# Performance work log

Measured on AMD Instinct MI355X. Metric: run time of the kernel, lower is better.

Reference implementation:

```python
import jax, jax.numpy as jnp
import numpy as np

N, C, H, W = 8, 80, 200, 200
PRE_NMS_THRESH = 0.05
PRE_NMS_TOP_N = 1000
NMS_THRESH = 0.6
FPN_POST_NMS_TOP_N = 100
MIN_SIZE = 0.0
TO_REMOVE = 1.0
CLASS_OFFSET = 100000.0  # > any coordinate; separates classes for class-aware NMS


def setup_inputs() -> dict:
    key = jax.random.key(0)
    k1, k2, k3, k4, k5 = jax.random.split(key, 5)
    # logits shifted so sigmoid probs sit near the 0.05 threshold (realistic sparsity)
    box_cls = jax.random.normal(k1, (N, C, H, W), jnp.float32) - 3.0
    box_regression = jax.random.uniform(k2, (N, 4, H, W), jnp.float32) * 64.0
    centerness = jax.random.normal(k3, (N, 1, H, W), jnp.float32)
    locations = jax.random.uniform(k4, (H * W, 2), jnp.float32) * 1600.0
    image_sizes = jax.random.randint(k5, (N, 2), 800, 1600, jnp.int32)  # (h, w)
    return {"locations": locations, "box_cls": box_cls,
            "box_regression": box_regression, "centerness": centerness,
            "image_sizes": image_sizes}


def _pairwise_iou(boxes):
    x1, y1, x2, y2 = boxes[:, 0], boxes[:, 1], boxes[:, 2], boxes[:, 3]
    area = (x2 - x1 + TO_REMOVE) * (y2 - y1 + TO_REMOVE)  # [K]
    iw = jnp.clip(jnp.minimum(x2[:, None], x2[None, :]) - jnp.maximum(x1[:, None], x1[None, :]) + TO_REMOVE, 0.0)
    ih = jnp.clip(jnp.minimum(y2[:, None], y2[None, :]) - jnp.maximum(y1[:, None], y1[None, :]) + TO_REMOVE, 0.0)
    inter = iw * ih
    return inter / (area[:, None] + area[None, :] - inter)


def reference(locations, box_cls, box_regression, centerness, image_sizes):
    n, c, h, w = box_cls.shape
    # [N,C,H,W] -> [N,HW,C] probs; [N,4,H,W] -> [N,HW,4]; centerness -> [N,HW]
    cls_prob = jax.nn.sigmoid(box_cls.transpose(0, 2, 3, 1).reshape(n, -1, c))
    reg = box_regression.transpose(0, 2, 3, 1).reshape(n, -1, 4)
    cent = jax.nn.sigmoid(centerness.transpose(0, 2, 3, 1).reshape(n, -1))

    def per_image(p, r, ct, hw):
        # candidate mask on raw class probs (before centerness weighting), as in source
        cand = p > PRE_NMS_THRESH                      # [HW, C]
        scores = p * ct[:, None]                       # [HW, C]
        flat = jnp.where(cand, scores, -jnp.inf).reshape(-1)
        top_s, top_i = jax.lax.top_k(flat, PRE_NMS_TOP_N)   # sorted desc
        loc_idx = top_i // c
        labels = top_i % c + 1
        valid = top_s > 0.0
        l2 = locations[loc_idx]                        # [K, 2]
        rr = r[loc_idx]                                # [K, 4]
        boxes = jnp.concatenate([l2 - rr[:, :2], l2 + rr[:, 2:]], axis=-1)
        ih = hw[0].astype(jnp.float32)
        iw = hw[1].astype(jnp.float32)
        boxes = jnp.stack([jnp.clip(boxes[:, 0], 0.0, iw - 1.0),
                           jnp.clip(boxes[:, 1], 0.0, ih - 1.0),
                           jnp.clip(boxes[:, 2], 0.0, iw - 1.0),
                           jnp.clip(boxes[:, 3], 0.0, ih - 1.0)], axis=-1)
        bw = boxes[:, 2] - boxes[:, 0] + TO_REMOVE
        bh = boxes[:, 3] - boxes[:, 1] + TO_REMOVE
        valid = valid & (bw >= MIN_SIZE) & (bh >= MIN_SIZE)
        # class-aware NMS via per-class coordinate offset
        ob = boxes + labels.astype(jnp.float32)[:, None] * CLASS_OFFSET
        iou = _pairwise_iou(ob)                        # [K, K]
        K = PRE_NMS_TOP_N
        idxs = jnp.arange(K)
        def body(supp, i):
            keep_i = valid[i] & jnp.logical_not(supp[i])
            supp = supp | (keep_i & (iou[i] > NMS_THRESH) & (idxs != i))
            return supp, keep_i
        _, keep = jax.lax.scan(body, jnp.zeros(K, dtype=bool), idxs)
        fscores = jnp.where(keep & valid, top_s, -jnp.inf)
        fs, fi = jax.lax.top_k(fscores, FPN_POST_NMS_TOP_N)
        fv = fs > 0.0
        fb = boxes[fi] * fv[:, None].astype(boxes.dtype)
        fl = jnp.where(fv, labels[fi], 0).astype(jnp.float32)
        out_s = jnp.where(fv, jnp.sqrt(jnp.where(fv, fs, 1.0)), 0.0)  # sqrt of cls*centerness
        # [K_post, 6] = x1,y1,x2,y2,score,label
        return jnp.concatenate([fb, out_s[:, None], fl[:, None]], axis=-1)

    return jax.vmap(per_image)(cls_prob, reg, cent, image_sizes)
```

## Files before the change

kernel.cpp:

```cpp
#include <hip/hip_runtime.h>
#include <math.h>

#define NIMG 8
#define NCLS 80
#define HW 40000
#define M (NCLS*HW)
#define UBINS 4096
#define CANDL 4096
#define SPILL_CAP 65536
#define BCAP 1024
#define TOPK 1000
#define OUTK 100
#define PRE_T 0.05f
#define NMS_T 0.6f
#define FLOOR_S 0.25f
#define FLOOR_BITS 0x3E800000u
#define FLOOR_SAFE 0.2494f

__device__ unsigned int       g_scnt[NIMG][32];
__device__ unsigned int       g_ovf[NIMG];
__device__ float              g_xthr[NIMG * HW];
__device__ float              g_sct[NIMG * HW];
__device__ unsigned long long g_key[NIMG][SPILL_CAP];

__device__ __forceinline__ float sigmoid_exact(float x){
    return 1.0f / (1.0f + expf(-x));
}

__global__ void k0_init(const float* __restrict__ cent){
    int t = blockIdx.x * blockDim.x + threadIdx.x;
    if (t < NIMG * 32) ((unsigned int*)g_scnt)[t] = 0u;
    if (t < NIMG) g_ovf[t] = 0u;
    if (t < NIMG * HW){
        float pct = sigmoid_exact(cent[t]);
        g_sct[t] = pct;
        float a = FLOOR_SAFE / pct;
        float xt;
        if (a >= 1.0f) xt = 3.0e38f;
        else {
            float am = fminf(a, 0.98f);
            xt = logf(am / (1.0f - am));
        }
        g_xthr[t] = xt;
    }
}

__global__ void __launch_bounds__(1024) k1_spill(const float* __restrict__ cls){
    const int n   = blockIdx.y;
    const int tid = threadIdx.x;
    const int e0  = blockIdx.x * 4096 + tid * 4;
    __shared__ unsigned long long skey[BCAP];
    __shared__ unsigned int lcnt, lbase;
    if (tid == 0) lcnt = 0u;
    __syncthreads();
    if (e0 < M){
        const int c  = e0 / HW;
        const int hw = e0 - c * HW;
        float4 x  = *(const float4*)(cls + (size_t)n * M + e0);
        float4 th = *(const float4*)(g_xthr + n * HW + hw);
        #define SPILL1(J, XV) \
        if (XV >= (J==0?th.x:J==1?th.y:J==2?th.z:th.w)){ \
            float p_ = sigmoid_exact(XV); \
            if (p_ > PRE_T){ \
                float s_ = p_ * g_sct[n * HW + hw + J]; \
                unsigned long long key_ = ((unsigned long long)__float_as_uint(s_) << 32) \
                    | (unsigned long long)(0xFFFFFFFFu - (unsigned int)((hw + J) * NCLS + c)); \
                unsigned int pp_ = atomicAdd(&lcnt, 1u); \
                if (pp_ < BCAP) skey[pp_] = key_; \
            } \
        }
        SPILL1(0, x.x)
        SPILL1(1, x.y)
        SPILL1(2, x.z)
        SPILL1(3, x.w)
        #undef SPILL1
    }
    __syncthreads();
    unsigned int raw = lcnt;
    unsigned int cnt = raw < BCAP ? raw : BCAP;
    if (tid == 0){
        lbase = cnt ? atomicAdd(&g_scnt[n][0], cnt) : 0u;
        if (raw > BCAP) g_ovf[n] = 1u;
    }
    __syncthreads();
    unsigned int base = lbase;
    for (unsigned int i = tid; i < cnt; i += 1024){
        unsigned int pos = base + i;
        if (pos < SPILL_CAP) g_key[n][pos] = skey[i];
    }
}

struct SelPhase {
    unsigned int hist[UBINS];
    unsigned int cs[256];
    unsigned long long keysL[CANDL];
};
struct NmsPhase {
    float ox1[TOPK], oy1[TOPK], ox2[TOPK], oy2[TOPK], oar[TOPK];
    float bxs[TOPK][4];
    float sc[TOPK];
    int   lab[TOPK];
    int   keeplist[OUTK];
    unsigned int  Wc[16][80];
    unsigned int  coff[81];
    unsigned int  wcnt[16];
    unsigned short ord[1024];
    unsigned char validf[TOPK];
    unsigned char supp[TOPK];
    unsigned char keepf[1024];
};
union KU { SelPhase sel; NmsPhase nms; };

__global__ void __launch_bounds__(1024) k2_select_nms(const float* __restrict__ cls,
                                                      const float* __restrict__ loc,
                                                      const float* __restrict__ reg,
                                                      const int*   __restrict__ imsz,
                                                      float* __restrict__ out){
    const int n = blockIdx.x;
    const int tid = threadIdx.x;
    const int lane = tid & 63;
    const int wv   = tid >> 6;
    __shared__ KU u;
    __shared__ unsigned long long stop[TOPK];
    __shared__ unsigned int lcnt, c025, s_cut, s_flag, s_nmsfb, s_cnt;

    for (int i = tid; i < UBINS; i += 1024) u.sel.hist[i] = 0u;
    if (tid == 0){ lcnt = 0u; c025 = 0u; s_nmsfb = 0u; }
    if (tid < TOPK) stop[tid] = 0ull;
    __syncthreads();

    unsigned int scnt_raw = g_scnt[n][0];
    unsigned int S = scnt_raw < SPILL_CAP ? scnt_raw : SPILL_CAP;

    for (unsigned int i = tid; i < S; i += 1024){
        unsigned long long k = g_key[n][i];
        unsigned int bits = (unsigned int)(k >> 32);
        float s = __uint_as_float(bits);
        int bin = (int)(s * 4096.0f);
        atomicAdd(&u.sel.hist[bin], 1u);
        unsigned long long mb = __ballot(bits >= FLOOR_BITS);
        if (lane == 0 && mb) atomicAdd(&c025, (unsigned int)__popcll(mb));
    }
    __syncthreads();
    if (tid < 256){
        unsigned int s = 0;
        int base = tid * 16;
        #pragma unroll
        for (int i = 0; i < 16; ++i) s += u.sel.hist[base + i];
        u.sel.cs[tid] = s;
    }
    __syncthreads();
    if (tid == 0){
        unsigned int acc = 0; int cut = 0;
        int c = 255;
        for (; c >= 0; --c){ if (acc + u.sel.cs[c] >= TOPK) break; acc += u.sel.cs[c]; }
        unsigned int Cest = 0;
        if (c >= 0){
            int b = c*16 + 15;
            for (;; --b){
                if (acc + u.sel.hist[b] >= TOPK || b == c*16){ cut = b; break; }
                acc += u.sel.hist[b];
            }
            Cest = acc + u.sel.hist[cut];
        }
        unsigned int fl = (scnt_raw > SPILL_CAP) || g_ovf[n] || (c < 0) ||
                          (c025 < TOPK) || (Cest > CANDL) ? 1u : 0u;
        s_cut = (unsigned int)cut; s_flag = fl;
    }
    __syncthreads();

    if (s_flag){
        for (int i = tid; i < UBINS; i += 1024) u.sel.hist[i] = 0u;
        __syncthreads();
        const float* cls_n = cls + (size_t)n * M;
        const float* sct_n = g_sct + n * HW;
        for (int e = tid; e < M; e += 1024){
            float p = sigmoid_exact(cls_n[e]);
            if (p > PRE_T){
                int c = e / HW; int hw = e - c * HW;
                float s = p * sct_n[hw];
                atomicAdd(&u.sel.hist[(int)(s * 4096.0f)], 1u);
            }
        }
        __syncthreads();
        if (tid < 256){
            unsigned int s = 0;
            int base = tid * 16;
            #pragma unroll
            for (int i = 0; i < 16; ++i) s += u.sel.hist[base + i];
            u.sel.cs[tid] = s;
        }
        __syncthreads();
        if (tid == 0){
            unsigned int acc = 0; int cut = 0; int c = 255;
            for (; c >= 0; --c){ if (acc + u.sel.cs[c] >= TOPK) break; acc += u.sel.cs[c]; }
            if (c >= 0){
                int b = c*16 + 15;
                for (;; --b){ acc += u.sel.hist[b]; if (acc >= TOPK || b == c*16) break; }
                cut = b;
            }
            while (acc > CANDL && cut < UBINS){ acc -= u.sel.hist[cut]; cut++; }
            s_cut = (unsigned int)cut;
        }
        __syncthreads();
        unsigned int cutb = s_cut;
        for (int e = tid; e < M; e += 1024){
            float p = sigmoid_exact(cls_n[e]);
            if (p > PRE_T){
                int c = e / HW; int hw = e - c * HW;
                float s = p * sct_n[hw];
                if ((int)(s * 4096.0f) >= (int)cutb){
                    unsigned int pos = atomicAdd(&lcnt, 1u);
                    if (pos < CANDL){
                        unsigned int idx = (unsigned int)(hw * NCLS + c);
                        u.sel.keysL[pos] = ((unsigned long long)__float_as_uint(s) << 32)
                                         | (unsigned long long)(0xFFFFFFFFu - idx);
                    }
                }
            }
        }
    } else {
        unsigned int cutb = s_cut;
        for (unsigned int i = tid; i < S; i += 1024){
            unsigned long long k = g_key[n][i];
            float s = __uint_as_float((unsigned int)(k >> 32));
            bool pass = ((unsigned int)(int)(s * 4096.0f)) >= cutb;
            unsigned long long mb = __ballot(pass);
            unsigned int wcnt_ = (unsigned int)__popcll(mb);
            unsigned int base = 0;
            if (lane == 0 && wcnt_) base = atomicAdd(&lcnt, wcnt_);
            base = (unsigned int)__builtin_amdgcn_readfirstlane((int)base);
            if (pass){
                unsigned int p = base + (unsigned int)__popcll(mb & ((1ull << lane) - 1ull));
                if (p < CANDL) u.sel.keysL[p] = k;
            }
        }
    }
    __syncthreads();

    int C = (int)(lcnt < CANDL ? lcnt : CANDL);
    if (C <= 2048){
        int Nsort = (C <= 1024) ? 1024 : 2048;
        for (int i = C + tid; i < Nsort; i += 1024) u.sel.keysL[i] = 0ull;
        __syncthreads();
        for (int k = 2; k <= Nsort; k <<= 1){
            for (int j = k >> 1; j > 0; j >>= 1){
                if (tid < (Nsort >> 1)){
                    int i  = ((tid & ~(j - 1)) << 1) | (tid & (j - 1));
                    int p2 = i | j;
                    unsigned long long a = u.sel.keysL[i];
                    unsigned long long b = u.sel.keysL[p2];
                    bool up = ((i & k) == 0);
                    if (up ? (a < b) : (a > b)){ u.sel.keysL[i] = b; u.sel.keysL[p2] = a; }
                }
                __syncthreads();
            }
        }
        if (tid < TOPK) stop[tid] = u.sel.keysL[tid];
    } else {
        for (int i = tid; i < C; i += 1024){
            unsigned long long k = u.sel.keysL[i];
            int rank = 0;
            for (int j = 0; j < C; ++j) rank += (u.sel.keysL[j] > k) ? 1 : 0;
            if (rank < TOPK) stop[rank] = k;
        }
    }
    __syncthreads();

    float rx1 = 0.f, ry1 = 0.f, rx2 = -1.f, ry2 = -1.f, rar = 1.f;
    float ihh = (float)imsz[2*n + 0];
    float iww = (float)imsz[2*n + 1];
    unsigned long long kk = (tid < TOPK) ? stop[tid] : 0ull;
    __syncthreads();

    u.nms.keepf[tid] = 0;
    { unsigned int* wz = &u.nms.Wc[0][0];
      for (int i = tid; i < 16*80; i += 1024) wz[i] = 0u; }

    if (tid < TOPK){
        unsigned int bits = (unsigned int)(kk >> 32);
        float s = __uint_as_float(bits);
        u.nms.supp[tid] = 0;
        if (s > 0.0f){
            unsigned int idx = 0xFFFFFFFFu - (unsigned int)(kk & 0xFFFFFFFFull);
            int hw = (int)(idx / NCLS);
            int c  = (int)(idx % NCLS);
            int l  = c + 1;
            float x  = loc[2*hw], y = loc[2*hw + 1];
            float r0 = reg[((size_t)n*4 + 0)*HW + hw];
            float r1 = reg[((size_t)n*4 + 1)*HW + hw];
            float r2 = reg[((size_t)n*4 + 2)*HW + hw];
            float r3 = reg[((size_t)n*4 + 3)*HW + hw];
            float x1 = fminf(fmaxf(x - r0, 0.0f), iww - 1.0f);
            float y1 = fminf(fmaxf(y - r1, 0.0f), ihh - 1.0f);
            float x2 = fminf(fmaxf(x + r2, 0.0f), iww - 1.0f);
            float y2 = fminf(fmaxf(y + r3, 0.0f), ihh - 1.0f);
            u.nms.bxs[tid][0] = x1; u.nms.bxs[tid][1] = y1;
            u.nms.bxs[tid][2] = x2; u.nms.bxs[tid][3] = y2;
            float off = (float)l * 100000.0f;
            float a1 = x1 + off, b1 = y1 + off, a2 = x2 + off, b2 = y2 + off;
            float ar = (a2 - a1 + 1.0f) * (b2 - b1 + 1.0f);
            u.nms.ox1[tid] = a1; u.nms.oy1[tid] = b1;
            u.nms.ox2[tid] = a2; u.nms.oy2[tid] = b2; u.nms.oar[tid] = ar;
            rx1 = a1; ry1 = b1; rx2 = a2; ry2 = b2; rar = ar;
            u.nms.sc[tid] = s; u.nms.lab[tid] = l; u.nms.validf[tid] = 1;
        } else {
            u.nms.validf[tid] = 0; u.nms.sc[tid] = 0.0f; u.nms.lab[tid] = 0;
            u.nms.bxs[tid][0] = u.nms.bxs[tid][1] = 0.0f;
            u.nms.bxs[tid][2] = u.nms.bxs[tid][3] = 0.0f;
            u.nms.ox1[tid] = 0.f; u.nms.oy1[tid] = 0.f;
            u.nms.ox2[tid] = -1.f; u.nms.oy2[tid] = -1.f; u.nms.oar[tid] = 1.f;
        }
    }
    __syncthreads();

    int mk = -1;
    if (tid < TOPK && u.nms.validf[tid]) mk = u.nms.lab[tid] - 1;
    if (mk >= 0) atomicAdd(&u.nms.Wc[wv][mk], 1u);
    __syncthreads();
    if (tid < NCLS){
        unsigned int acc = 0;
        for (int w = 0; w < 16; ++w){
            unsigned int v = u.nms.Wc[w][tid];
            u.nms.Wc[w][tid] = acc;
            acc += v;
        }
        u.nms.coff[tid] = acc;
        if (acc > 64) atomicOr(&s_nmsfb, 1u);
    }
    __syncthreads();
    if (tid == 0){
        unsigned int acc = 0;
        for (int k = 0; k < NCLS; ++k){ unsigned int t = u.nms.coff[k]; u.nms.coff[k] = acc; acc += t; }
        u.nms.coff[NCLS] = acc;
    }
    __syncthreads();

    if (!s_nmsfb){
        int below = 0;
        for (int l = 0; l < 64; ++l){
            int ok = __shfl(mk, l);
            below += (l < lane && ok == mk) ? 1 : 0;
        }
        if (mk >= 0){
            unsigned int pos = u.nms.coff[mk] + u.nms.Wc[wv][mk] + (unsigned int)below;
            u.nms.ord[pos] = (unsigned short)tid;
        }
        __syncthreads();

        for (int k = wv; k < NCLS; k += 16){
            int base = (int)u.nms.coff[k];
            int ck   = (int)u.nms.coff[k + 1] - base;
            if (ck <= 0) continue;
            int rr = (lane < ck) ? (int)u.nms.ord[base + lane] : -1;
            float bx1 = 0.f, by1 = 0.f, bx2 = -1.f, by2 = -1.f, bar = 1.f;
            if (rr >= 0){
                bx1 = u.nms.ox1[rr]; by1 = u.nms.oy1[rr];
                bx2 = u.nms.ox2[rr]; by2 = u.nms.oy2[rr]; bar = u.nms.oar[rr];
            }
            int sup = 0;
            for (int p = 0; p < ck; ++p){
                int keep_p = !__shfl(sup, p);
                if (keep_p){
                    float px1 = __shfl(bx1, p), py1 = __shfl(by1, p);
                    float px2 = __shfl(bx2, p), py2 = __shfl(by2, p);
                    float par = __shfl(bar, p);
                    if (lane > p && rr >= 0){
                        float ix1 = fmaxf(px1, bx1);
                        float iy1 = fmaxf(py1, by1);
                        float ix2 = fminf(px2, bx2);
                        float iy2 = fminf(py2, by2);
                        float iw_ = fmaxf(ix2 - ix1 + 1.0f, 0.0f);
                        float ih_ = fmaxf(iy2 - iy1 + 1.0f, 0.0f);
                        float inter = iw_ * ih_;
                        float iou = inter / (par + bar - inter);
                        if (iou > NMS_T) sup = 1;
                    }
                }
            }
            if (rr >= 0) u.nms.keepf[rr] = sup ? 0 : 1;
        }
        __syncthreads();

        int kf = (int)u.nms.keepf[tid];
        unsigned long long mb = __ballot(kf != 0);
        if (lane == 0) u.nms.wcnt[wv] = (unsigned int)__popcll(mb);
        __syncthreads();
        if (tid == 0){
            unsigned int acc = 0;
            for (int w = 0; w < 16; ++w){ unsigned int t = u.nms.wcnt[w]; u.nms.wcnt[w] = acc; acc += t; }
            s_cnt = acc < OUTK ? acc : OUTK;
        }
        __syncthreads();
        if (kf){
            unsigned int slot = u.nms.wcnt[wv] + (unsigned int)__popcll(mb & ((1ull << lane) - 1ull));
            if (slot < OUTK) u.nms.keeplist[slot] = tid;
        }
    } else {
        int cnt = 0;
        for (int i = 0; i < TOPK; ++i){
            bool keep_i = u.nms.validf[i] && !u.nms.supp[i];
            if (keep_i){
                if (tid == 0) u.nms.keeplist[cnt] = i;
                if (tid < TOPK && tid != i){
                    float ix1 = fmaxf(u.nms.ox1[i], rx1);
                    float iy1 = fmaxf(u.nms.oy1[i], ry1);
                    float ix2 = fminf(u.nms.ox2[i], rx2);
                    float iy2 = fminf(u.nms.oy2[i], ry2);
                    float iw_ = fmaxf(ix2 - ix1 + 1.0f, 0.0f);
                    float ih_ = fmaxf(iy2 - iy1 + 1.0f, 0.0f);
                    float inter = iw_ * ih_;
                    float iou = inter / (u.nms.oar[i] + rar - inter);
                    if (iou > NMS_T) u.nms.supp[tid] = 1;
                }
                cnt++;
                __syncthreads();
                if (cnt == OUTK) break;
            }
        }
        if (tid == 0) s_cnt = (unsigned int)(cnt < OUTK ? cnt : OUTK);
    }
    __syncthreads();

    int cnt = (int)s_cnt;
    if (tid < OUTK){
        float r0=0.f,r1=0.f,r2=0.f,r3=0.f,r4=0.f,r5=0.f;
        if (tid < cnt){
            int i = u.nms.keeplist[tid];
            r0 = u.nms.bxs[i][0]; r1 = u.nms.bxs[i][1];
            r2 = u.nms.bxs[i][2]; r3 = u.nms.bxs[i][3];
            r4 = sqrtf(u.nms.sc[i]); r5 = (float)u.nms.lab[i];
        }
        float* o = out + ((size_t)n*OUTK + tid)*6;
        o[0]=r0; o[1]=r1; o[2]=r2; o[3]=r3; o[4]=r4; o[5]=r5;
    }
}

extern "C" void kernel_launch(void* const* d_in, const int* in_sizes, int n_in,
                              void* d_out, int out_size, void* d_ws, size_t ws_size,
                              hipStream_t stream){
    const float* loc  = (const float*)d_in[0];
    const float* cls  = (const float*)d_in[1];
    const float* reg  = (const float*)d_in[2];
    const float* cent = (const float*)d_in[3];
    const int*   imsz = (const int*)d_in[4];
    float* out = (float*)d_out;

    hipLaunchKernelGGL(k0_init,       dim3(625),                 dim3(512),  0, stream, cent);
    hipLaunchKernelGGL(k1_spill,      dim3((M+4095)/4096, NIMG), dim3(1024), 0, stream, cls);
    hipLaunchKernelGGL(k2_select_nms, dim3(NIMG),                dim3(1024), 0, stream,
                       cls, loc, reg, imsz, out);
}
```

Baseline: 257.4 us.

## Add direct register bitonic sort fast path and wave-aggregated spill

The spill kernel drops its per-block shared-memory staging and instead uses wave ballots with one global atomic per wave, writing keys straight to the global buffer. The select kernel gains a fast path: when the spill count is between 1000 and 2048 with no overflow, it sorts all spilled keys directly using a bitonic sort that does the small strides with register shuffles and only the larger strides in shared memory. This skips the histogram and cut passes whenever the 1000th key still clears the floor. Several serial single-thread prefix scans are also replaced with parallel or shuffle-based scans. The cost is more global atomics in the spill kernel and extra shuffle work, in exchange for fewer barriers and fewer passes over the keys.

```diff
diff --git a/kernel.cpp b/kernel.cpp
--- a/kernel.cpp
+++ b/kernel.cpp
@@ -8,7 +8,6 @@
 #define UBINS 4096
 #define CANDL 4096
 #define SPILL_CAP 65536
-#define BCAP 1024
 #define TOPK 1000
 #define OUTK 100
 #define PRE_T 0.05f
@@ -25,6 +24,12 @@
 
 __device__ __forceinline__ float sigmoid_exact(float x){
     return 1.0f / (1.0f + expf(-x));
+}
+
+__device__ __forceinline__ unsigned long long shfl_xor_u64(unsigned long long v, int j){
+    int lo = __shfl_xor((int)(unsigned int)(v & 0xffffffffull), j);
+    int hi = __shfl_xor((int)(unsigned int)(v >> 32), j);
+    return ((unsigned long long)(unsigned int)hi << 32) | (unsigned long long)(unsigned int)lo;
 }
 
 __global__ void k0_init(const float* __restrict__ cent){
@@ -46,48 +51,43 @@
 }
 
 __global__ void __launch_bounds__(1024) k1_spill(const float* __restrict__ cls){
-    const int n   = blockIdx.y;
-    const int tid = threadIdx.x;
-    const int e0  = blockIdx.x * 4096 + tid * 4;
-    __shared__ unsigned long long skey[BCAP];
-    __shared__ unsigned int lcnt, lbase;
-    if (tid == 0) lcnt = 0u;
-    __syncthreads();
-    if (e0 < M){
-        const int c  = e0 / HW;
-        const int hw = e0 - c * HW;
-        float4 x  = *(const float4*)(cls + (size_t)n * M + e0);
-        float4 th = *(const float4*)(g_xthr + n * HW + hw);
-        #define SPILL1(J, XV) \
-        if (XV >= (J==0?th.x:J==1?th.y:J==2?th.z:th.w)){ \
+    const int n    = blockIdx.y;
+    const int tid  = threadIdx.x;
+    const int lane = tid & 63;
+    const int e0   = blockIdx.x * 4096 + tid * 4;
+    if (e0 >= M) return;
+    const int c  = e0 / HW;
+    const int hw = e0 - c * HW;
+    float4 x  = *(const float4*)(cls + (size_t)n * M + e0);
+    float4 th = *(const float4*)(g_xthr + n * HW + hw);
+    #define SPILLW(J, XV, TH) { \
+        bool cd2 = false; unsigned long long key_ = 0ull; \
+        if (XV >= TH){ \
             float p_ = sigmoid_exact(XV); \
             if (p_ > PRE_T){ \
                 float s_ = p_ * g_sct[n * HW + hw + J]; \
-                unsigned long long key_ = ((unsigned long long)__float_as_uint(s_) << 32) \
-                    | (unsigned long long)(0xFFFFFFFFu - (unsigned int)((hw + J) * NCLS + c)); \
-                unsigned int pp_ = atomicAdd(&lcnt, 1u); \
-                if (pp_ < BCAP) skey[pp_] = key_; \
+                key_ = ((unsigned long long)__float_as_uint(s_) << 32) \
+                     | (unsigned long long)(0xFFFFFFFFu - (unsigned int)((hw + J) * NCLS + c)); \
+                cd2 = true; \
             } \
-        }
-        SPILL1(0, x.x)
-        SPILL1(1, x.y)
-        SPILL1(2, x.z)
-        SPILL1(3, x.w)
-        #undef SPILL1
-    }
-    __syncthreads();
-    unsigned int raw = lcnt;
-    unsigned int cnt = raw < BCAP ? raw : BCAP;
-    if (tid == 0){
-        lbase = cnt ? atomicAdd(&g_scnt[n][0], cnt) : 0u;
-        if (raw > BCAP) g_ovf[n] = 1u;
-    }
-    __syncthreads();
-    unsigned int base = lbase;
-    for (unsigned int i = tid; i < cnt; i += 1024){
-        unsigned int pos = base + i;
-        if (pos < SPILL_CAP) g_key[n][pos] = skey[i];
-    }
+        } \
+        unsigned long long mk_ = __ballot(cd2); \
+        if (mk_){ \
+            unsigned int base_ = 0; \
+            if (lane == 0) base_ = atomicAdd(&g_scnt[n][0], (unsigned int)__popcll(mk_)); \
+            base_ = (unsigned int)__builtin_amdgcn_readfirstlane((int)base_); \
+            if (cd2){ \
+                unsigned int pos_ = base_ + (unsigned int)__popcll(mk_ & ((1ull << lane) - 1ull)); \
+                if (pos_ < SPILL_CAP) g_key[n][pos_] = key_; \
+                else g_ovf[n] = 1u; \
+            } \
+        } \
+    }
+    SPILLW(0, x.x, th.x)
+    SPILLW(1, x.y, th.y)
+    SPILLW(2, x.z, th.z)
+    SPILLW(3, x.w, th.w)
+    #undef SPILLW
 }
 
 struct SelPhase {
@@ -102,6 +102,7 @@
     int   lab[TOPK];
     int   keeplist[OUTK];
     unsigned int  Wc[16][80];
+    unsigned int  ctot[80];
     unsigned int  coff[81];
     unsigned int  wcnt[16];
     unsigned short ord[1024];
@@ -110,6 +111,16 @@
     unsigned char keepf[1024];
 };
 union KU { SelPhase sel; NmsPhase nms; };
+
+#define REGSTEP(K_, J_) { \
+    unsigned long long pa = shfl_xor_u64(va, (J_)); \
+    unsigned long long pb = shfl_xor_u64(vb, (J_)); \
+    bool fa = ((tid & (J_)) == 0); \
+    bool da = ((tid & (K_)) == 0); \
+    bool db = (((tid + 1024) & (K_)) == 0); \
+    va = (fa == da) ? (va > pa ? va : pa) : (va < pa ? va : pa); \
+    vb = (fa == db) ? (vb > pb ? vb : pb) : (vb < pb ? vb : pb); \
+}
 
 __global__ void __launch_bounds__(1024) k2_select_nms(const float* __restrict__ cls,
                                                       const float* __restrict__ loc,
@@ -122,65 +133,69 @@
     const int wv   = tid >> 6;
     __shared__ KU u;
     __shared__ unsigned long long stop[TOPK];
-    __shared__ unsigned int lcnt, c025, s_cut, s_flag, s_nmsfb, s_cnt;
-
-    for (int i = tid; i < UBINS; i += 1024) u.sel.hist[i] = 0u;
-    if (tid == 0){ lcnt = 0u; c025 = 0u; s_nmsfb = 0u; }
-    if (tid < TOPK) stop[tid] = 0ull;
-    __syncthreads();
+    __shared__ unsigned int lcnt, c025, s_cut, s_flag, s_nmsfb, s_cnt, s_aok;
+
+    if (tid == 0){ s_nmsfb = 0u; }
 
     unsigned int scnt_raw = g_scnt[n][0];
+    unsigned int ovf_f    = g_ovf[n];
     unsigned int S = scnt_raw < SPILL_CAP ? scnt_raw : SPILL_CAP;
 
-    for (unsigned int i = tid; i < S; i += 1024){
-        unsigned long long k = g_key[n][i];
-        unsigned int bits = (unsigned int)(k >> 32);
-        float s = __uint_as_float(bits);
-        int bin = (int)(s * 4096.0f);
-        atomicAdd(&u.sel.hist[bin], 1u);
-        unsigned long long mb = __ballot(bits >= FLOOR_BITS);
-        if (lane == 0 && mb) atomicAdd(&c025, (unsigned int)__popcll(mb));
-    }
-    __syncthreads();
-    if (tid < 256){
-        unsigned int s = 0;
-        int base = tid * 16;
-        #pragma unroll
-        for (int i = 0; i < 16; ++i) s += u.sel.hist[base + i];
-        u.sel.cs[tid] = s;
-    }
-    __syncthreads();
-    if (tid == 0){
-        unsigned int acc = 0; int cut = 0;
-        int c = 255;
-        for (; c >= 0; --c){ if (acc + u.sel.cs[c] >= TOPK) break; acc += u.sel.cs[c]; }
-        unsigned int Cest = 0;
-        if (c >= 0){
-            int b = c*16 + 15;
-            for (;; --b){
-                if (acc + u.sel.hist[b] >= TOPK || b == c*16){ cut = b; break; }
-                acc += u.sel.hist[b];
-            }
-            Cest = acc + u.sel.hist[cut];
-        }
-        unsigned int fl = (scnt_raw > SPILL_CAP) || g_ovf[n] || (c < 0) ||
-                          (c025 < TOPK) || (Cest > CANDL) ? 1u : 0u;
-        s_cut = (unsigned int)cut; s_flag = fl;
-    }
-    __syncthreads();
-
-    if (s_flag){
+    bool modeA = (!ovf_f) && (scnt_raw >= TOPK) && (scnt_raw <= 2048);
+    unsigned long long kk = 0ull;
+    bool needBC = true;
+
+    if (modeA){
+        unsigned long long va = ((unsigned int)tid < S) ? g_key[n][tid] : 0ull;
+        unsigned long long vb = ((unsigned int)(tid + 1024) < S) ? g_key[n][tid + 1024] : 0ull;
+
+        REGSTEP(2,1)
+        REGSTEP(4,2)  REGSTEP(4,1)
+        REGSTEP(8,4)  REGSTEP(8,2)  REGSTEP(8,1)
+        REGSTEP(16,8) REGSTEP(16,4) REGSTEP(16,2) REGSTEP(16,1)
+        REGSTEP(32,16) REGSTEP(32,8) REGSTEP(32,4) REGSTEP(32,2) REGSTEP(32,1)
+        REGSTEP(64,32) REGSTEP(64,16) REGSTEP(64,8) REGSTEP(64,4) REGSTEP(64,2) REGSTEP(64,1)
+
+        for (int k = 128; k <= 2048; k <<= 1){
+            if (k == 2048){
+                unsigned long long mx = va > vb ? va : vb;
+                unsigned long long mn = va > vb ? vb : va;
+                va = mx; vb = mn;
+            }
+            u.sel.keysL[tid] = va; u.sel.keysL[tid + 1024] = vb;
+            __syncthreads();
+            for (int j = (k == 2048) ? 512 : (k >> 1); j >= 64; j >>= 1){
+                int i  = ((tid & ~(j - 1)) << 1) | (tid & (j - 1));
+                int l  = i | j;
+                unsigned long long a = u.sel.keysL[i];
+                unsigned long long b = u.sel.keysL[l];
+                bool up = ((i & k) == 0);
+                if (up ? (a < b) : (a > b)){ u.sel.keysL[i] = b; u.sel.keysL[l] = a; }
+                __syncthreads();
+            }
+            va = u.sel.keysL[tid]; vb = u.sel.keysL[tid + 1024];
+            REGSTEP(k,32) REGSTEP(k,16) REGSTEP(k,8) REGSTEP(k,4) REGSTEP(k,2) REGSTEP(k,1)
+        }
+        if (tid == TOPK - 1) s_aok = (((unsigned int)(va >> 32)) >= FLOOR_BITS) ? 1u : 0u;
+        kk = (tid < TOPK) ? va : 0ull;
+        __syncthreads();
+        needBC = (s_aok == 0u);
+    }
+
+    if (needBC){
         for (int i = tid; i < UBINS; i += 1024) u.sel.hist[i] = 0u;
-        __syncthreads();
-        const float* cls_n = cls + (size_t)n * M;
-        const float* sct_n = g_sct + n * HW;
-        for (int e = tid; e < M; e += 1024){
-            float p = sigmoid_exact(cls_n[e]);
-            if (p > PRE_T){
-                int c = e / HW; int hw = e - c * HW;
-                float s = p * sct_n[hw];
-                atomicAdd(&u.sel.hist[(int)(s * 4096.0f)], 1u);
-            }
+        if (tid == 0){ lcnt = 0u; c025 = 0u; }
+        if (tid < TOPK) stop[tid] = 0ull;
+        __syncthreads();
+
+        for (unsigned int i = tid; i < S; i += 1024){
+            unsigned long long k = g_key[n][i];
+            unsigned int bits = (unsigned int)(k >> 32);
+            float s = __uint_as_float(bits);
+            int bin = (int)(s * 4096.0f);
+            atomicAdd(&u.sel.hist[bin], 1u);
+            unsigned long long mb = __ballot(bits >= FLOOR_BITS);
+            if (lane == 0 && mb) atomicAdd(&c025, (unsigned int)__popcll(mb));
         }
         __syncthreads();
         if (tid < 256){
@@ -192,86 +207,128 @@
         }
         __syncthreads();
         if (tid == 0){
-            unsigned int acc = 0; int cut = 0; int c = 255;
+            unsigned int acc = 0; int cut = 0;
+            int c = 255;
             for (; c >= 0; --c){ if (acc + u.sel.cs[c] >= TOPK) break; acc += u.sel.cs[c]; }
+            unsigned int Cest = 0;
             if (c >= 0){
                 int b = c*16 + 15;
-                for (;; --b){ acc += u.sel.hist[b]; if (acc >= TOPK || b == c*16) break; }
-                cut = b;
-            }
-            while (acc > CANDL && cut < UBINS){ acc -= u.sel.hist[cut]; cut++; }
-            s_cut = (unsigned int)cut;
-        }
-        __syncthreads();
-        unsigned int cutb = s_cut;
-        for (int e = tid; e < M; e += 1024){
-            float p = sigmoid_exact(cls_n[e]);
-            if (p > PRE_T){
-                int c = e / HW; int hw = e - c * HW;
-                float s = p * sct_n[hw];
-                if ((int)(s * 4096.0f) >= (int)cutb){
-                    unsigned int pos = atomicAdd(&lcnt, 1u);
-                    if (pos < CANDL){
-                        unsigned int idx = (unsigned int)(hw * NCLS + c);
-                        u.sel.keysL[pos] = ((unsigned long long)__float_as_uint(s) << 32)
-                                         | (unsigned long long)(0xFFFFFFFFu - idx);
+                for (;; --b){
+                    if (acc + u.sel.hist[b] >= TOPK || b == c*16){ cut = b; break; }
+                    acc += u.sel.hist[b];
+                }
+                Cest = acc + u.sel.hist[cut];
+            }
+            unsigned int fl = (scnt_raw > SPILL_CAP) || ovf_f || (c < 0) ||
+                              (c025 < TOPK) || (Cest > CANDL) ? 1u : 0u;
+            s_cut = (unsigned int)cut; s_flag = fl;
+        }
+        __syncthreads();
+
+        if (s_flag){
+            for (int i = tid; i < UBINS; i += 1024) u.sel.hist[i] = 0u;
+            __syncthreads();
+            const float* cls_n = cls + (size_t)n * M;
+            const float* sct_n = g_sct + n * HW;
+            for (int e = tid; e < M; e += 1024){
+                float p = sigmoid_exact(cls_n[e]);
+                if (p > PRE_T){
+                    int c = e / HW; int hw = e - c * HW;
+                    float s = p * sct_n[hw];
+                    atomicAdd(&u.sel.hist[(int)(s * 4096.0f)], 1u);
+                }
+            }
+            __syncthreads();
+            if (tid < 256){
+                unsigned int s = 0;
+                int base = tid * 16;
+                #pragma unroll
+                for (int i = 0; i < 16; ++i) s += u.sel.hist[base + i];
+                u.sel.cs[tid] = s;
+            }
+            __syncthreads();
+            if (tid == 0){
+                unsigned int acc = 0; int cut = 0; int c = 255;
+                for (; c >= 0; --c){ if (acc + u.sel.cs[c] >= TOPK) break; acc += u.sel.cs[c]; }
+                if (c >= 0){
+                    int b = c*16 + 15;
+                    for (;; --b){ acc += u.sel.hist[b]; if (acc >= TOPK || b == c*16) break; }
+                    cut = b;
+                }
+                while (acc > CANDL && cut < UBINS){ acc -= u.sel.hist[cut]; cut++; }
+                s_cut = (unsigned int)cut;
+            }
+            __syncthreads();
+            unsigned int cutb = s_cut;
+            for (int e = tid; e < M; e += 1024){
+                float p = sigmoid_exact(cls_n[e]);
+                if (p > PRE_T){
+                    int c = e / HW; int hw = e - c * HW;
+                    float s = p * sct_n[hw];
+                    if ((int)(s * 4096.0f) >= (int)cutb){
+                        unsigned int pos = atomicAdd(&lcnt, 1u);
+                        if (pos < CANDL){
+                            unsigned int idx = (unsigned int)(hw * NCLS + c);
+                            u.sel.keysL[pos] = ((unsigned long long)__float_as_uint(s) << 32)
+                                             | (unsigned long long)(0xFFFFFFFFu - idx);
+                        }
                     }
                 }
             }
-        }
-    } else {
-        unsigned int cutb = s_cut;
-        for (unsigned int i = tid; i < S; i += 1024){
-            unsigned long long k = g_key[n][i];
-            float s = __uint_as_float((unsigned int)(k >> 32));
-            bool pass = ((unsigned int)(int)(s * 4096.0f)) >= cutb;
-            unsigned long long mb = __ballot(pass);
-            unsigned int wcnt_ = (unsigned int)__popcll(mb);
-            unsigned int base = 0;
-            if (lane == 0 && wcnt_) base = atomicAdd(&lcnt, wcnt_);
-            base = (unsigned int)__builtin_amdgcn_readfirstlane((int)base);
-            if (pass){
-                unsigned int p = base + (unsigned int)__popcll(mb & ((1ull << lane) - 1ull));
-                if (p < CANDL) u.sel.keysL[p] = k;
-            }
-        }
-    }
-    __syncthreads();
-
-    int C = (int)(lcnt < CANDL ? lcnt : CANDL);
-    if (C <= 2048){
-        int Nsort = (C <= 1024) ? 1024 : 2048;
-        for (int i = C + tid; i < Nsort; i += 1024) u.sel.keysL[i] = 0ull;
-        __syncthreads();
-        for (int k = 2; k <= Nsort; k <<= 1){
-            for (int j = k >> 1; j > 0; j >>= 1){
-                if (tid < (Nsort >> 1)){
-                    int i  = ((tid & ~(j - 1)) << 1) | (tid & (j - 1));
-                    int p2 = i | j;
-                    unsigned long long a = u.sel.keysL[i];
-                    unsigned long long b = u.sel.keysL[p2];
-                    bool up = ((i & k) == 0);
-                    if (up ? (a < b) : (a > b)){ u.sel.keysL[i] = b; u.sel.keysL[p2] = a; }
-                }
-                __syncthreads();
-            }
-        }
-        if (tid < TOPK) stop[tid] = u.sel.keysL[tid];
-    } else {
-        for (int i = tid; i < C; i += 1024){
-            unsigned long long k = u.sel.keysL[i];
-            int rank = 0;
-            for (int j = 0; j < C; ++j) rank += (u.sel.keysL[j] > k) ? 1 : 0;
-            if (rank < TOPK) stop[rank] = k;
-        }
-    }
-    __syncthreads();
+        } else {
+            unsigned int cutb = s_cut;
+            for (unsigned int i = tid; i < S; i += 1024){
+                unsigned long long k = g_key[n][i];
+                float s = __uint_as_float((unsigned int)(k >> 32));
+                bool pass = ((unsigned int)(int)(s * 4096.0f)) >= cutb;
+                unsigned long long mb = __ballot(pass);
+                unsigned int wcnt_ = (unsigned int)__popcll(mb);
+                unsigned int base = 0;
+                if (lane == 0 && wcnt_) base = atomicAdd(&lcnt, wcnt_);
+                base = (unsigned int)__builtin_amdgcn_readfirstlane((int)base);
+                if (pass){
+                    unsigned int p = base + (unsigned int)__popcll(mb & ((1ull << lane) - 1ull));
+                    if (p < CANDL) u.sel.keysL[p] = k;
+                }
+            }
+        }
+        __syncthreads();
+
+        int C = (int)(lcnt < CANDL ? lcnt : CANDL);
+        if (C <= 2048){
+            int Nsort = (C <= 1024) ? 1024 : 2048;
+            for (int i = C + tid; i < Nsort; i += 1024) u.sel.keysL[i] = 0ull;
+            __syncthreads();
+            for (int k = 2; k <= Nsort; k <<= 1){
+                for (int j = k >> 1; j > 0; j >>= 1){
+                    if (tid < (Nsort >> 1)){
+                        int i  = ((tid & ~(j - 1)) << 1) | (tid & (j - 1));
+                        int p2 = i | j;
+                        unsigned long long a = u.sel.keysL[i];
+                        unsigned long long b = u.sel.keysL[p2];
+                        bool up = ((i & k) == 0);
+                        if (up ? (a < b) : (a > b)){ u.sel.keysL[i] = b; u.sel.keysL[p2] = a; }
+                    }
+                    __syncthreads();
+                }
+            }
+            if (tid < TOPK) stop[tid] = u.sel.keysL[tid];
+        } else {
+            for (int i = tid; i < C; i += 1024){
+                unsigned long long k = u.sel.keysL[i];
+                int rank = 0;
+                for (int j = 0; j < C; ++j) rank += (u.sel.keysL[j] > k) ? 1 : 0;
+                if (rank < TOPK) stop[rank] = k;
+            }
+        }
+        __syncthreads();
+        kk = (tid < TOPK) ? stop[tid] : 0ull;
+        __syncthreads();
+    }
 
     float rx1 = 0.f, ry1 = 0.f, rx2 = -1.f, ry2 = -1.f, rar = 1.f;
     float ihh = (float)imsz[2*n + 0];
     float iww = (float)imsz[2*n + 1];
-    unsigned long long kk = (tid < TOPK) ? stop[tid] : 0ull;
-    __syncthreads();
 
     u.nms.keepf[tid] = 0;
     { unsigned int* wz = &u.nms.Wc[0][0];
@@ -325,14 +382,14 @@
             u.nms.Wc[w][tid] = acc;
             acc += v;
         }
+        u.nms.ctot[tid] = acc;
+        if (acc > 64) atomicOr(&s_nmsfb, 1u);
+    }
+    __syncthreads();
+    if (tid <= NCLS){
+        unsigned int acc = 0;
+        for (int kq = 0; kq < tid; ++kq) acc += u.nms.ctot[kq];
         u.nms.coff[tid] = acc;
-        if (acc > 64) atomicOr(&s_nmsfb, 1u);
-    }
-    __syncthreads();
-    if (tid == 0){
-        unsigned int acc = 0;
-        for (int k = 0; k < NCLS; ++k){ unsigned int t = u.nms.coff[k]; u.nms.coff[k] = acc; acc += t; }
-        u.nms.coff[NCLS] = acc;
     }
     __syncthreads();
 
@@ -386,10 +443,15 @@
         unsigned long long mb = __ballot(kf != 0);
         if (lane == 0) u.nms.wcnt[wv] = (unsigned int)__popcll(mb);
         __syncthreads();
-        if (tid == 0){
-            unsigned int acc = 0;
-            for (int w = 0; w < 16; ++w){ unsigned int t = u.nms.wcnt[w]; u.nms.wcnt[w] = acc; acc += t; }
-            s_cnt = acc < OUTK ? acc : OUTK;
+        if (wv == 0){
+            unsigned int v = (lane < 16) ? u.nms.wcnt[lane] : 0u;
+            unsigned int orig = v;
+            for (int d = 1; d < 16; d <<= 1){
+                unsigned int t = __shfl_up(v, d);
+                if (lane >= d) v += t;
+            }
+            if (lane < 16) u.nms.wcnt[lane] = v - orig;
+            if (lane == 15) s_cnt = (v < OUTK ? v : OUTK);
         }
         __syncthreads();
         if (kf){
```

Result: slower. 847.2 us (+229.2%).
